# Kernel optimization log

Measured on AMD Instinct MI355X. Metric: run time of the kernel, lower is better.

## Reference

```python
import jax, jax.numpy as jnp
import numpy as np

N_NODES = 100000
N_EDGES = 1600000
D_IN = 128
D_OUT = 128


def setup_inputs() -> dict:
    key = jax.random.key(0)
    k1, k2, k3, k4, k5 = jax.random.split(key, 5)
    h = jax.random.normal(k1, (N_NODES, D_IN), dtype=jnp.float32)
    src = jax.random.randint(k2, (N_EDGES,), 0, N_NODES, dtype=jnp.int64)
    dst = jax.random.randint(k3, (N_EDGES,), 0, N_NODES, dtype=jnp.int64)
    W = jax.random.normal(k4, (2 * D_IN, D_OUT), dtype=jnp.float32) * (1.0 / np.sqrt(2 * D_IN))
    b = jax.random.normal(k5, (D_OUT,), dtype=jnp.float32) * 0.01
    return {"h": h, "src": src, "dst": dst, "W": W, "b": b}


def reference(h, src, dst, W, b):
    # copy_u + mean: scatter-mean of source features onto destination nodes
    msg_sum = jax.ops.segment_sum(h[src], dst, num_segments=N_NODES)  # [N, D_IN]
    deg = jax.ops.segment_sum(jnp.ones((src.shape[0],), h.dtype), dst, num_segments=N_NODES)  # [N]
    h_N = jnp.where(deg[:, None] > 0, msg_sum / jnp.maximum(deg, 1.0)[:, None], 0.0)
    h_total = jnp.concatenate([h, h_N], axis=1)  # [N, 2*D_IN]
    return h_total @ W + b
```

## Files before the change

kernel.cpp:

```cpp
#include <hip/hip_runtime.h>
#include <stdint.h>

#define N_NODES 100000
#define D 128
#define BN 64
#define NB ((N_NODES + BN - 1) / BN)
#define EPB 8192
#define CAP 1536

typedef short bf16x8 __attribute__((ext_vector_type(8)));
typedef float f32x4 __attribute__((ext_vector_type(4)));

__device__ __forceinline__ float bf2f(unsigned short u) {
    return __uint_as_float(((unsigned int)u) << 16);
}
__device__ __forceinline__ unsigned short f2bf(float f) {
    unsigned int x = __float_as_uint(f);
    unsigned int r = x + 0x7fffu + ((x >> 16) & 1u);
    return (unsigned short)(r >> 16);
}

__global__ __launch_bounds__(256) void prep_k(
    const float* __restrict__ h, unsigned short* __restrict__ h_bf,
    const float* __restrict__ W, unsigned short* __restrict__ Wf,
    const int* __restrict__ src, const int* __restrict__ dst,
    int* __restrict__ cnt, unsigned int* __restrict__ pairs,
    int n_edges, int part_blocks)
{
    __shared__ int hist[NB];
    __shared__ int gbase[NB];
    __shared__ int lc[NB];

    int bid = blockIdx.x;
    int t = threadIdx.x;

    if (bid < part_blocks) {
        for (int i = t; i < NB; i += 256) { hist[i] = 0; lc[i] = 0; }
        __syncthreads();
        int base = bid * EPB;
        int lim = n_edges - base; if (lim > EPB) lim = EPB;
        for (int i = t; i < lim; i += 256)
            atomicAdd(&hist[dst[base + i] >> 6], 1);
        __syncthreads();
        for (int i = t; i < NB; i += 256) {
            int c = hist[i];
            gbase[i] = c ? atomicAdd(&cnt[i], c) : 0;
        }
        __syncthreads();
        for (int i = t; i < lim; i += 256) {
            int e = base + i;
            int d = dst[e], b = d >> 6;
            int slot = atomicAdd(&lc[b], 1);
            int off = gbase[b] + slot;
            if (off < CAP)
                pairs[(size_t)b * CAP + off] =
                    (unsigned int)src[e] | ((unsigned int)(d & 63) << 17);
        }
    } else if (bid < part_blocks + 16) {
        int gid = (bid - part_blocks) * 256 + t;
        if (gid < 64 * 64) {
            int f = gid >> 6, l = gid & 63;
            int kt = f >> 3, ct = f & 7;
            int n = ct * 16 + (l & 15);
            int kb = kt * 32 + (l >> 4) * 8;
            #pragma unroll
            for (int j = 0; j < 8; ++j)
                Wf[(size_t)f * 512 + l * 8 + j] = f2bf(W[(size_t)(kb + j) * D + n]);
        }
    } else {
        size_t base = ((size_t)(bid - part_blocks - 16) * 256 + t) * 4;
        if (base < (size_t)N_NODES * D) {
            float4 v = *(const float4*)(h + base);
            ushort4 o;
            o.x = f2bf(v.x); o.y = f2bf(v.y); o.z = f2bf(v.z); o.w = f2bf(v.w);
            *(ushort4*)(h_bf + base) = o;
        }
    }
}

__global__ __launch_bounds__(512, 8) void agg3_k(
    const unsigned short* __restrict__ h_bf, const unsigned int* __restrict__ pairs,
    const int* __restrict__ cnt_g, unsigned short* __restrict__ hN_bf)
{
    __shared__ unsigned int lp[CAP];
    __shared__ unsigned int srt[CAP];
    __shared__ int counts[BN];
    __shared__ int startp[BN];
    __shared__ int cursor[BN];

    int t = threadIdx.x;
    int b = blockIdx.x;
    size_t e0 = (size_t)b * CAP;
    int cnt = cnt_g[b];
    if (cnt > CAP) cnt = CAP;

    if (t < BN) counts[t] = 0;
    __syncthreads();

    for (int i = t; i < cnt; i += 512) {
        unsigned int p = pairs[e0 + i];
        lp[i] = p;
        atomicAdd(&counts[p >> 17], 1);
    }
    __syncthreads();

    if (t < BN) startp[t] = counts[t];
    __syncthreads();
    #pragma unroll
    for (int off = 1; off < BN; off <<= 1) {
        int v = 0;
        if (t < BN && t >= off) v = startp[t - off];
        __syncthreads();
        if (t < BN) startp[t] += v;
        __syncthreads();
    }
    if (t < BN) {
        int ex = startp[t] - counts[t];
        startp[t] = ex;
        cursor[t] = ex;
    }
    __syncthreads();

    for (int i = t; i < cnt; i += 512) {
        unsigned int p = lp[i];
        int s = atomicAdd(&cursor[p >> 17], 1);
        srt[s] = p & 0x1FFFFu;
    }
    __syncthreads();

    int wv = t >> 6, l = t & 63;
    int half = l >> 5, j = l & 31;
    int nbase = b * BN;
    for (int nl = wv; nl < BN; nl += 8) {
        int n = nbase + nl;
        if (n >= N_NODES) break;
        int dg = counts[nl], s0 = startp[nl];
        float a0 = 0.f, a1 = 0.f, a2 = 0.f, a3 = 0.f;
        int e = 0;
        for (; e + 8 <= dg; e += 8) {
            int r0 = srt[s0 + e     + half];
            int r1 = srt[s0 + e + 2 + half];
            int r2 = srt[s0 + e + 4 + half];
            int r3 = srt[s0 + e + 6 + half];
            uint2 u0 = *(const uint2*)(h_bf + (size_t)r0 * D + j * 4);
            uint2 u1 = *(const uint2*)(h_bf + (size_t)r1 * D + j * 4);
            uint2 u2 = *(const uint2*)(h_bf + (size_t)r2 * D + j * 4);
            uint2 u3 = *(const uint2*)(h_bf + (size_t)r3 * D + j * 4);
            a0 += (__uint_as_float(u0.x << 16) + __uint_as_float(u1.x << 16))
                + (__uint_as_float(u2.x << 16) + __uint_as_float(u3.x << 16));
            a1 += (__uint_as_float(u0.x & 0xffff0000u) + __uint_as_float(u1.x & 0xffff0000u))
                + (__uint_as_float(u2.x & 0xffff0000u) + __uint_as_float(u3.x & 0xffff0000u));
            a2 += (__uint_as_float(u0.y << 16) + __uint_as_float(u1.y << 16))
                + (__uint_as_float(u2.y << 16) + __uint_as_float(u3.y << 16));
            a3 += (__uint_as_float(u0.y & 0xffff0000u) + __uint_as_float(u1.y & 0xffff0000u))
                + (__uint_as_float(u2.y & 0xffff0000u) + __uint_as_float(u3.y & 0xffff0000u));
        }
        for (; e + 2 <= dg; e += 2) {
            int r = srt[s0 + e + half];
            uint2 u = *(const uint2*)(h_bf + (size_t)r * D + j * 4);
            a0 += __uint_as_float(u.x << 16);
            a1 += __uint_as_float(u.x & 0xffff0000u);
            a2 += __uint_as_float(u.y << 16);
            a3 += __uint_as_float(u.y & 0xffff0000u);
        }
        if (e < dg) {
            int r = srt[s0 + e];
            uint2 u = *(const uint2*)(h_bf + (size_t)r * D + j * 4);
            float m = half ? 0.f : 1.f;
            a0 += m * __uint_as_float(u.x << 16);
            a1 += m * __uint_as_float(u.x & 0xffff0000u);
            a2 += m * __uint_as_float(u.y << 16);
            a3 += m * __uint_as_float(u.y & 0xffff0000u);
        }
        a0 += __shfl_xor(a0, 32);
        a1 += __shfl_xor(a1, 32);
        a2 += __shfl_xor(a2, 32);
        a3 += __shfl_xor(a3, 32);
        float invd = dg > 0 ? 1.0f / (float)dg : 0.f;
        if (half == 0) {
            uint2 o;
            o.x = ((unsigned int)f2bf(a1 * invd) << 16) | f2bf(a0 * invd);
            o.y = ((unsigned int)f2bf(a3 * invd) << 16) | f2bf(a2 * invd);
            *(uint2*)(hN_bf + (size_t)n * D + j * 4) = o;
        }
    }
}

__global__ __launch_bounds__(256) void gemm_k(
    const unsigned short* __restrict__ h_bf, const unsigned short* __restrict__ hN_bf,
    const unsigned short* __restrict__ Wf, const float* __restrict__ bias,
    float* __restrict__ out)
{
    int tid = threadIdx.x;
    int w = tid >> 6, l = tid & 63;
    int n0 = blockIdx.x * 128 + w * 32;
    int lrow = l & 15, lq = l >> 4;

    int r0 = n0 + lrow;      if (r0 > N_NODES - 1) r0 = N_NODES - 1;
    int r1 = n0 + 16 + lrow; if (r1 > N_NODES - 1) r1 = N_NODES - 1;

    f32x4 acc[2][8];
    #pragma unroll
    for (int rg = 0; rg < 2; ++rg)
        #pragma unroll
        for (int ct = 0; ct < 8; ++ct)
            acc[rg][ct] = (f32x4){0.f, 0.f, 0.f, 0.f};

    const unsigned short* wf_lane = Wf + l * 8;

    #pragma unroll
    for (int kt = 0; kt < 8; ++kt) {
        const unsigned short* Abase = (kt < 4) ? h_bf : hN_bf;
        int ko = (kt & 3) * 32 + lq * 8;
        bf16x8 a0 = *(const bf16x8*)(Abase + (size_t)r0 * D + ko);
        bf16x8 a1 = *(const bf16x8*)(Abase + (size_t)r1 * D + ko);
        #pragma unroll
        for (int ct = 0; ct < 8; ++ct) {
            bf16x8 bfr = *(const bf16x8*)(wf_lane + (size_t)(kt * 8 + ct) * 512);
            acc[0][ct] = __builtin_amdgcn_mfma_f32_16x16x32_bf16(a0, bfr, acc[0][ct], 0, 0, 0);
            acc[1][ct] = __builtin_amdgcn_mfma_f32_16x16x32_bf16(a1, bfr, acc[1][ct], 0, 0, 0);
        }
    }

    int col = l & 15, q = l >> 4;
    #pragma unroll
    for (int ct = 0; ct < 8; ++ct) {
        float bv = bias[ct * 16 + col];
        #pragma unroll
        for (int rg = 0; rg < 2; ++rg) {
            #pragma unroll
            for (int r = 0; r < 4; ++r) {
                int row = n0 + rg * 16 + q * 4 + r;
                if (row < N_NODES)
                    out[(size_t)row * D + ct * 16 + col] = acc[rg][ct][r] + bv;
            }
        }
    }
}


extern "C" void kernel_launch(void* const* d_in, const int* in_sizes, int n_in,
                              void* d_out, int out_size, void* d_ws, size_t ws_size,
                              hipStream_t stream) {
    const float* h  = (const float*)d_in[0];
    const int* src  = (const int*)d_in[1];
    const int* dst  = (const int*)d_in[2];
    const float* W  = (const float*)d_in[3];
    const float* b  = (const float*)d_in[4];
    float* out      = (float*)d_out;
    int n_edges = in_sizes[1];

    char* ws = (char*)d_ws;
    unsigned short* h_bf  = (unsigned short*)ws;
    unsigned short* hN_bf = h_bf + (size_t)N_NODES * D;
    unsigned int* pairs   = (unsigned int*)(hN_bf + (size_t)N_NODES * D);
    unsigned short* Wf    = (unsigned short*)(pairs + (size_t)NB * CAP);
    int* cnt              = (int*)(Wf + 64 * 512);

    hipMemsetAsync(cnt, 0, NB * sizeof(int), stream);

    int pb = (n_edges + EPB - 1) / EPB;
    int cblocks = (int)(((size_t)N_NODES * D / 4 + 255) / 256);
    hipLaunchKernelGGL(prep_k, dim3(pb + 16 + cblocks), dim3(256), 0, stream,
                       h, h_bf, W, Wf, src, dst, cnt, pairs, n_edges, pb);

    hipLaunchKernelGGL(agg3_k, dim3(NB), dim3(512), 0, stream,
                       h_bf, pairs, cnt, hN_bf);
    hipLaunchKernelGGL(gemm_k, dim3((N_NODES + 127) / 128), dim3(256), 0, stream,
                       h_bf, hN_bf, Wf, b, out);
}
```

Before: 261.3 us.

## Fuse aggregation with GEMM via LDS and replace edge partitioning with global atomics

The mean-aggregation and GEMM kernels are merged. Each aggregation block keeps its 64-node neighbor means in shared memory and immediately multiplies them with W, so the hN_bf round trip through global memory and one launch are gone. The edge-bucketing pass drops the per-block shared histogram and instead does one global atomicAdd per edge, spread across the h-conversion blocks. This costs many more contended global atomics and a smaller per-block GEMM tile (4 MFMA chains per wave).

```diff
diff --git a/kernel.cpp b/kernel.cpp
--- a/kernel.cpp
+++ b/kernel.cpp
@@ -5,15 +5,12 @@
 #define D 128
 #define BN 64
 #define NB ((N_NODES + BN - 1) / BN)
-#define EPB 8192
 #define CAP 1536
+#define HPAD 136
 
 typedef short bf16x8 __attribute__((ext_vector_type(8)));
 typedef float f32x4 __attribute__((ext_vector_type(4)));
 
-__device__ __forceinline__ float bf2f(unsigned short u) {
-    return __uint_as_float(((unsigned int)u) << 16);
-}
 __device__ __forceinline__ unsigned short f2bf(float f) {
     unsigned int x = __float_as_uint(f);
     unsigned int r = x + 0x7fffu + ((x >> 16) & 1u);
@@ -25,39 +22,31 @@
     const float* __restrict__ W, unsigned short* __restrict__ Wf,
     const int* __restrict__ src, const int* __restrict__ dst,
     int* __restrict__ cnt, unsigned int* __restrict__ pairs,
-    int n_edges, int part_blocks)
+    int n_edges, int cblocks, int epb)
 {
-    __shared__ int hist[NB];
-    __shared__ int gbase[NB];
-    __shared__ int lc[NB];
-
     int bid = blockIdx.x;
     int t = threadIdx.x;
 
-    if (bid < part_blocks) {
-        for (int i = t; i < NB; i += 256) { hist[i] = 0; lc[i] = 0; }
-        __syncthreads();
-        int base = bid * EPB;
-        int lim = n_edges - base; if (lim > EPB) lim = EPB;
-        for (int i = t; i < lim; i += 256)
-            atomicAdd(&hist[dst[base + i] >> 6], 1);
-        __syncthreads();
-        for (int i = t; i < NB; i += 256) {
-            int c = hist[i];
-            gbase[i] = c ? atomicAdd(&cnt[i], c) : 0;
-        }
-        __syncthreads();
-        for (int i = t; i < lim; i += 256) {
-            int e = base + i;
-            int d = dst[e], b = d >> 6;
-            int slot = atomicAdd(&lc[b], 1);
-            int off = gbase[b] + slot;
-            if (off < CAP)
-                pairs[(size_t)b * CAP + off] =
-                    (unsigned int)src[e] | ((unsigned int)(d & 63) << 17);
-        }
-    } else if (bid < part_blocks + 16) {
-        int gid = (bid - part_blocks) * 256 + t;
+    if (bid < cblocks) {
+        size_t base = ((size_t)bid * 256 + t) * 4;
+        float4 v = *(const float4*)(h + base);
+
+        for (int i = t; i < epb; i += 256) {
+            int e = bid * epb + i;
+            if (e < n_edges) {
+                int d = dst[e], b = d >> 6;
+                int slot = atomicAdd(&cnt[b], 1);
+                if (slot < CAP)
+                    pairs[(size_t)b * CAP + slot] =
+                        (unsigned int)src[e] | ((unsigned int)(d & 63) << 17);
+            }
+        }
+
+        ushort4 o;
+        o.x = f2bf(v.x); o.y = f2bf(v.y); o.z = f2bf(v.z); o.w = f2bf(v.w);
+        *(ushort4*)(h_bf + base) = o;
+    } else {
+        int gid = (bid - cblocks) * 256 + t;
         if (gid < 64 * 64) {
             int f = gid >> 6, l = gid & 63;
             int kt = f >> 3, ct = f & 7;
@@ -67,26 +56,20 @@
             for (int j = 0; j < 8; ++j)
                 Wf[(size_t)f * 512 + l * 8 + j] = f2bf(W[(size_t)(kb + j) * D + n]);
         }
-    } else {
-        size_t base = ((size_t)(bid - part_blocks - 16) * 256 + t) * 4;
-        if (base < (size_t)N_NODES * D) {
-            float4 v = *(const float4*)(h + base);
-            ushort4 o;
-            o.x = f2bf(v.x); o.y = f2bf(v.y); o.z = f2bf(v.z); o.w = f2bf(v.w);
-            *(ushort4*)(h_bf + base) = o;
-        }
-    }
-}
-
-__global__ __launch_bounds__(512, 8) void agg3_k(
+    }
+}
+
+__global__ __launch_bounds__(512, 8) void aggemm_k(
     const unsigned short* __restrict__ h_bf, const unsigned int* __restrict__ pairs,
-    const int* __restrict__ cnt_g, unsigned short* __restrict__ hN_bf)
+    const int* __restrict__ cnt_g, const unsigned short* __restrict__ Wf,
+    const float* __restrict__ bias, float* __restrict__ out)
 {
     __shared__ unsigned int lp[CAP];
     __shared__ unsigned int srt[CAP];
     __shared__ int counts[BN];
     __shared__ int startp[BN];
     __shared__ int cursor[BN];
+    __shared__ unsigned short hNs[BN][HPAD];
 
     int t = threadIdx.x;
     int b = blockIdx.x;
@@ -181,59 +164,49 @@
             uint2 o;
             o.x = ((unsigned int)f2bf(a1 * invd) << 16) | f2bf(a0 * invd);
             o.y = ((unsigned int)f2bf(a3 * invd) << 16) | f2bf(a2 * invd);
-            *(uint2*)(hN_bf + (size_t)n * D + j * 4) = o;
-        }
-    }
-}
-
-__global__ __launch_bounds__(256) void gemm_k(
-    const unsigned short* __restrict__ h_bf, const unsigned short* __restrict__ hN_bf,
-    const unsigned short* __restrict__ Wf, const float* __restrict__ bias,
-    float* __restrict__ out)
-{
-    int tid = threadIdx.x;
-    int w = tid >> 6, l = tid & 63;
-    int n0 = blockIdx.x * 128 + w * 32;
+            *(uint2*)(&hNs[nl][j * 4]) = o;
+        }
+    }
+    __syncthreads();
+
+    int w = t >> 6;
+    int rt = w >> 1, ch = w & 1;
     int lrow = l & 15, lq = l >> 4;
-
-    int r0 = n0 + lrow;      if (r0 > N_NODES - 1) r0 = N_NODES - 1;
-    int r1 = n0 + 16 + lrow; if (r1 > N_NODES - 1) r1 = N_NODES - 1;
-
-    f32x4 acc[2][8];
-    #pragma unroll
-    for (int rg = 0; rg < 2; ++rg)
+    int lr = rt * 16 + lrow;
+    int r0 = nbase + lr; if (r0 > N_NODES - 1) r0 = N_NODES - 1;
+
+    f32x4 acc[4];
+    #pragma unroll
+    for (int c = 0; c < 4; ++c) acc[c] = (f32x4){0.f, 0.f, 0.f, 0.f};
+
+    const unsigned short* wf_lane = Wf + l * 8;
+
+    #pragma unroll
+    for (int kt = 0; kt < 8; ++kt) {
+        int ko = (kt & 3) * 32 + lq * 8;
+        bf16x8 a;
+        if (kt < 4)
+            a = *(const bf16x8*)(h_bf + (size_t)r0 * D + ko);
+        else
+            a = *(const bf16x8*)(&hNs[lr][ko]);
         #pragma unroll
-        for (int ct = 0; ct < 8; ++ct)
-            acc[rg][ct] = (f32x4){0.f, 0.f, 0.f, 0.f};
-
-    const unsigned short* wf_lane = Wf + l * 8;
-
-    #pragma unroll
-    for (int kt = 0; kt < 8; ++kt) {
-        const unsigned short* Abase = (kt < 4) ? h_bf : hN_bf;
-        int ko = (kt & 3) * 32 + lq * 8;
-        bf16x8 a0 = *(const bf16x8*)(Abase + (size_t)r0 * D + ko);
-        bf16x8 a1 = *(const bf16x8*)(Abase + (size_t)r1 * D + ko);
-        #pragma unroll
-        for (int ct = 0; ct < 8; ++ct) {
+        for (int c = 0; c < 4; ++c) {
+            int ct = ch * 4 + c;
             bf16x8 bfr = *(const bf16x8*)(wf_lane + (size_t)(kt * 8 + ct) * 512);
-            acc[0][ct] = __builtin_amdgcn_mfma_f32_16x16x32_bf16(a0, bfr, acc[0][ct], 0, 0, 0);
-            acc[1][ct] = __builtin_amdgcn_mfma_f32_16x16x32_bf16(a1, bfr, acc[1][ct], 0, 0, 0);
+            acc[c] = __builtin_amdgcn_mfma_f32_16x16x32_bf16(a, bfr, acc[c], 0, 0, 0);
         }
     }
 
     int col = l & 15, q = l >> 4;
     #pragma unroll
-    for (int ct = 0; ct < 8; ++ct) {
+    for (int c = 0; c < 4; ++c) {
+        int ct = ch * 4 + c;
         float bv = bias[ct * 16 + col];
         #pragma unroll
-        for (int rg = 0; rg < 2; ++rg) {
-            #pragma unroll
-            for (int r = 0; r < 4; ++r) {
-                int row = n0 + rg * 16 + q * 4 + r;
-                if (row < N_NODES)
-                    out[(size_t)row * D + ct * 16 + col] = acc[rg][ct][r] + bv;
-            }
+        for (int r = 0; r < 4; ++r) {
+            int row = nbase + rt * 16 + q * 4 + r;
+            if (row < N_NODES)
+                out[(size_t)row * D + ct * 16 + col] = acc[c][r] + bv;
         }
     }
 }
@@ -252,20 +225,17 @@
 
     char* ws = (char*)d_ws;
     unsigned short* h_bf  = (unsigned short*)ws;
-    unsigned short* hN_bf = h_bf + (size_t)N_NODES * D;
-    unsigned int* pairs   = (unsigned int*)(hN_bf + (size_t)N_NODES * D);
+    unsigned int* pairs   = (unsigned int*)(h_bf + (size_t)N_NODES * D);
     unsigned short* Wf    = (unsigned short*)(pairs + (size_t)NB * CAP);
     int* cnt              = (int*)(Wf + 64 * 512);
 
     hipMemsetAsync(cnt, 0, NB * sizeof(int), stream);
 
-    int pb = (n_edges + EPB - 1) / EPB;
     int cblocks = (int)(((size_t)N_NODES * D / 4 + 255) / 256);
-    hipLaunchKernelGGL(prep_k, dim3(pb + 16 + cblocks), dim3(256), 0, stream,
-                       h, h_bf, W, Wf, src, dst, cnt, pairs, n_edges, pb);
-
-    hipLaunchKernelGGL(agg3_k, dim3(NB), dim3(512), 0, stream,
-                       h_bf, pairs, cnt, hN_bf);
-    hipLaunchKernelGGL(gemm_k, dim3((N_NODES + 127) / 128), dim3(256), 0, stream,
-                       h_bf, hN_bf, Wf, b, out);
-}
+    int epb = (n_edges + cblocks - 1) / cblocks;
+    hipLaunchKernelGGL(prep_k, dim3(cblocks + 16), dim3(256), 0, stream,
+                       h, h_bf, W, Wf, src, dst, cnt, pairs, n_edges, cblocks, epb);
+
+    hipLaunchKernelGGL(aggemm_k, dim3(NB), dim3(512), 0, stream,
+                       h_bf, pairs, cnt, Wf, b, out);
+}
```

Measured after the change: 418.4 us. 60.1% more time.
